# Kernel tuning notes

Measured on AMD Instinct MI355X. Metric: run time of the kernel, lower is better.

## Reference

```python
import jax, jax.numpy as jnp
import numpy as np

N = 50000      # nodes per graph batch (per siamese side)
E = 500000     # edges per side
F_IN = 128     # input_channels
H = 128        # hidden_channels
OUT = 2        # output_channels
G = 512        # number of graphs in the batch


def setup_inputs() -> dict:
    key = jax.random.key(0)
    ks = jax.random.split(key, 16)

    def lin_w(k, fan_in, shape):
        lim = 1.0 / np.sqrt(fan_in)
        return jax.random.uniform(k, shape, jnp.float32, -lim, lim)

    return {
        "x1": jax.random.normal(ks[0], (N, F_IN), jnp.float32),
        "x2": jax.random.normal(ks[1], (N, F_IN), jnp.float32),
        "edge_index1": jax.random.randint(ks[2], (2, E), 0, N, jnp.int32),
        "edge_index2": jax.random.randint(ks[3], (2, E), 0, N, jnp.int32),
        "batch1": jnp.sort(jax.random.randint(ks[4], (N,), 0, G, jnp.int32)),
        "batch2": jnp.sort(jax.random.randint(ks[5], (N,), 0, G, jnp.int32)),
        "W1": lin_w(ks[6], F_IN, (F_IN, H)), "b1": jnp.zeros((H,), jnp.float32),
        "W2": lin_w(ks[7], H, (H, H)),       "b2": jnp.zeros((H,), jnp.float32),
        "W3": lin_w(ks[8], H, (H, H)),       "b3": jnp.zeros((H,), jnp.float32),
        "Wc1": lin_w(ks[9], 2 * H, (2 * H, 4 * H)), "bc1": jnp.zeros((4 * H,), jnp.float32),
        "Wc2": lin_w(ks[10], 4 * H, (4 * H, 2 * H)), "bc2": jnp.zeros((2 * H,), jnp.float32),
        "Wc3": lin_w(ks[11], 2 * H, (2 * H, OUT)),   "bc3": jnp.zeros((OUT,), jnp.float32),
        "num_graphs": G,
    }


def _gcn_layer(x, W, b, src, dst, dinv):
    # PyG GCNConv: linear transform, then deg^{-1/2} A_hat deg^{-1/2} aggregation + bias
    h = x @ W
    msg = h[src] * (dinv[src] * dinv[dst])[:, None]   # [E+N, H]
    return jax.ops.segment_sum(msg, dst, num_segments=x.shape[0]) + b


def _forward_once(x, edge_index, batch, W1, b1, W2, b2, W3, b3, num_graphs):
    n = x.shape[0]
    loop = jnp.arange(n, dtype=edge_index.dtype)
    src = jnp.concatenate([edge_index[0], loop])      # add self-loops
    dst = jnp.concatenate([edge_index[1], loop])
    deg = jax.ops.segment_sum(jnp.ones_like(dst, dtype=x.dtype), dst, num_segments=n)
    dinv = jax.lax.rsqrt(deg)                          # deg >= 1 due to self-loops
    h = jax.nn.relu(_gcn_layer(x, W1, b1, src, dst, dinv))
    h = jax.nn.relu(_gcn_layer(h, W2, b2, src, dst, dinv))
    h = _gcn_layer(h, W3, b3, src, dst, dinv)
    # global_mean_pool over batch indices
    s = jax.ops.segment_sum(h, batch, num_segments=num_graphs)
    cnt = jax.ops.segment_sum(jnp.ones((n,), x.dtype), batch, num_segments=num_graphs)
    return s / jnp.maximum(cnt, 1.0)[:, None]


def reference(x1, x2, edge_index1, edge_index2, batch1, batch2,
              W1, b1, W2, b2, W3, b3, Wc1, bc1, Wc2, bc2, Wc3, bc3, num_graphs):
    g1 = _forward_once(x1, edge_index1, batch1, W1, b1, W2, b2, W3, b3, num_graphs)
    g2 = _forward_once(x2, edge_index2, batch2, W1, b1, W2, b2, W3, b3, num_graphs)
    z = jnp.concatenate([g1, g2], axis=1)             # [G, 2H]
    z = jax.nn.relu(z @ Wc1 + bc1)
    z = jax.nn.relu(z @ Wc2 + bc2)
    # dropout p=0.5 is identity at eval time
    return z @ Wc3 + bc3                               # [G, OUT]
```

## Files before the change

kernel.cpp:

```cpp
#include <hip/hip_runtime.h>
#include <math.h>

#define N_NODES 50000
#define E_EDGES 500000
#define HDIM    128
#define OUTC    2
#define NGRAPH  512

typedef _Float16 f16x8 __attribute__((ext_vector_type(8)));
typedef float    f32x4 __attribute__((ext_vector_type(4)));

__global__ void k_prep(int* __restrict__ zA, int nA, int* __restrict__ zB, int nB,
                       const float* __restrict__ W1, const float* __restrict__ W2,
                       _Float16* __restrict__ w1hi, _Float16* __restrict__ w1lo,
                       _Float16* __restrict__ w2hi, _Float16* __restrict__ w2lo) {
    int i = blockIdx.x * blockDim.x + threadIdx.x;
    int stride = gridDim.x * blockDim.x;
    for (int j = i; j < nA; j += stride) zA[j] = 0;
    for (int j = i; j < nB; j += stride) zB[j] = 0;
    for (int j = i; j < 128 * 128; j += stride) {
        int n = j >> 7, k = j & 127;
        float v = W1[k * 128 + n];
        _Float16 h = (_Float16)v;
        w1hi[j] = h; w1lo[j] = (_Float16)(v - (float)h);
        v = W2[k * 128 + n];
        h = (_Float16)v;
        w2hi[j] = h; w2lo[j] = (_Float16)(v - (float)h);
    }
}

__global__ void k_hist(const int* __restrict__ d0, const int* __restrict__ d1,
                       int ecnt, int off1, int* __restrict__ cnt) {
    int i = blockIdx.x * blockDim.x + threadIdx.x;
    int stride = gridDim.x * blockDim.x;
    for (; i < ecnt; i += stride) {
        int d = (i < E_EDGES) ? d0[i] : d1[i - E_EDGES] + off1;
        atomicAdd(&cnt[d], 1);
    }
}

__global__ void k_scan_a(const int* __restrict__ cnt, int* __restrict__ excl,
                         int* __restrict__ blksum, float* __restrict__ dinv,
                         const int* __restrict__ bt0, const int* __restrict__ bt1,
                         int goff0, int nn, int nside, float* __restrict__ cnt_g) {
    __shared__ int s[512];
    int t = threadIdx.x;
    int i = blockIdx.x * 512 + t;
    int v = 0;
    if (i < nn) {
        v = cnt[i];
        dinv[i] = 1.0f / sqrtf((float)(v + 1));
        int g = (i < nside) ? bt0[i] + goff0 : bt1[i - nside] + NGRAPH;
        atomicAdd(&cnt_g[g], 1.0f);
    }
    s[t] = v; __syncthreads();
    for (int off = 1; off < 512; off <<= 1) {
        int add = (t >= off) ? s[t - off] : 0;
        __syncthreads();
        s[t] += add;
        __syncthreads();
    }
    if (i < nn) excl[i] = s[t] - v;
    if (t == 511) blksum[blockIdx.x] = s[511];
}

__global__ void k_scan_b(int* __restrict__ blksum, int nb) {
    __shared__ int s[512];
    int t = threadIdx.x;
    int v = (t < nb) ? blksum[t] : 0;
    s[t] = v; __syncthreads();
    for (int off = 1; off < 512; off <<= 1) {
        int add = (t >= off) ? s[t - off] : 0;
        __syncthreads();
        s[t] += add;
        __syncthreads();
    }
    if (t < nb) blksum[t] = s[t] - v;
}

__global__ void k_scan_c(int* __restrict__ excl, const int* __restrict__ blksum,
                         int nn, int tot) {
    int t = threadIdx.x;
    int i = blockIdx.x * 512 + t;
    if (i < nn) excl[i] += blksum[blockIdx.x];
    if (i == 0) excl[nn] = tot;
}

__global__ void k_fill(const int* __restrict__ s0, const int* __restrict__ s1,
                       const int* __restrict__ d0, const int* __restrict__ d1,
                       int ecnt, int off1,
                       const int* __restrict__ row_ptr, int* __restrict__ fill_cnt,
                       const float* __restrict__ dinv, int2* __restrict__ edges) {
    int i = blockIdx.x * blockDim.x + threadIdx.x;
    int stride = gridDim.x * blockDim.x;
    for (; i < ecnt; i += stride) {
        int d, sg;
        if (i < E_EDGES) { sg = s0[i]; d = d0[i]; }
        else             { sg = s1[i - E_EDGES] + off1; d = d1[i - E_EDGES] + off1; }
        int p = atomicAdd(&fill_cnt[d], 1);
        float w = dinv[sg] * dinv[d];
        edges[row_ptr[d] + p] = make_int2(sg, __float_as_int(w));
    }
}

__device__ inline void cvt8(const float4& p, const float4& q, f16x8& h, f16x8& l) {
    float v[8] = {p.x, p.y, p.z, p.w, q.x, q.y, q.z, q.w};
#pragma unroll
    for (int i = 0; i < 8; i++) {
        _Float16 hh = (_Float16)v[i];
        h[i] = hh;
        l[i] = (_Float16)(v[i] - (float)hh);
    }
}

template <int ASRC>
__global__ __launch_bounds__(256) void k_gemm_split(
        const float* __restrict__ A0f, const float* __restrict__ A1f, int nside,
        const _Float16* __restrict__ Ahi, const _Float16* __restrict__ Alo,
        const _Float16* __restrict__ Bhi, const _Float16* __restrict__ Blo,
        float* __restrict__ C, int M) {
    __shared__ _Float16 sA[2][128][40];
    __shared__ _Float16 sB[2][128][40];
    int tid = threadIdx.x;
    int wave = tid >> 6, lane = tid & 63;
    int wm = (wave >> 1) * 64;
    int wn = (wave & 1) * 64;
    int quad = lane >> 4, fm = lane & 15;
    int row0 = blockIdx.x * 128;

    int lr = tid >> 2;
    int lk = (tid & 3) * 8;

    f32x4 acc[4][4] = {};
    const float4 z4 = make_float4(0.f, 0.f, 0.f, 0.f);

    for (int kc = 0; kc < 128; kc += 32) {
        int r1 = row0 + lr, r2 = row0 + lr + 64;
        bool ok1 = r1 < M, ok2 = r2 < M;
        f16x8 ah1, al1, ah2, al2;
        if (ASRC == 1) {
            const float* p1 = (r1 < nside) ? A0f + (size_t)r1 * 128
                                           : A1f + (size_t)(r1 - nside) * 128;
            const float* p2 = (r2 < nside) ? A0f + (size_t)r2 * 128
                                           : A1f + (size_t)(r2 - nside) * 128;
            float4 a = ok1 ? *(const float4*)(p1 + kc + lk) : z4;
            float4 b = ok1 ? *(const float4*)(p1 + kc + lk + 4) : z4;
            float4 c = ok2 ? *(const float4*)(p2 + kc + lk) : z4;
            float4 d = ok2 ? *(const float4*)(p2 + kc + lk + 4) : z4;
            cvt8(a, b, ah1, al1);
            cvt8(c, d, ah2, al2);
        } else {
            const f16x8 zf = {};
            ah1 = ok1 ? *(const f16x8*)(Ahi + (size_t)r1 * 128 + kc + lk) : zf;
            al1 = ok1 ? *(const f16x8*)(Alo + (size_t)r1 * 128 + kc + lk) : zf;
            ah2 = ok2 ? *(const f16x8*)(Ahi + (size_t)r2 * 128 + kc + lk) : zf;
            al2 = ok2 ? *(const f16x8*)(Alo + (size_t)r2 * 128 + kc + lk) : zf;
        }
        f16x8 bh1 = *(const f16x8*)(Bhi + (size_t)lr * 128 + kc + lk);
        f16x8 bl1 = *(const f16x8*)(Blo + (size_t)lr * 128 + kc + lk);
        f16x8 bh2 = *(const f16x8*)(Bhi + (size_t)(lr + 64) * 128 + kc + lk);
        f16x8 bl2 = *(const f16x8*)(Blo + (size_t)(lr + 64) * 128 + kc + lk);
        __syncthreads();
        *(f16x8*)&sA[0][lr][lk]      = ah1;
        *(f16x8*)&sA[1][lr][lk]      = al1;
        *(f16x8*)&sA[0][lr + 64][lk] = ah2;
        *(f16x8*)&sA[1][lr + 64][lk] = al2;
        *(f16x8*)&sB[0][lr][lk]      = bh1;
        *(f16x8*)&sB[1][lr][lk]      = bl1;
        *(f16x8*)&sB[0][lr + 64][lk] = bh2;
        *(f16x8*)&sB[1][lr + 64][lk] = bl2;
        __syncthreads();

        f16x8 afh[4], afl[4], bfh[4], bfl[4];
#pragma unroll
        for (int mi = 0; mi < 4; mi++) {
            afh[mi] = *(const f16x8*)&sA[0][wm + mi * 16 + fm][quad * 8];
            afl[mi] = *(const f16x8*)&sA[1][wm + mi * 16 + fm][quad * 8];
        }
#pragma unroll
        for (int ni = 0; ni < 4; ni++) {
            bfh[ni] = *(const f16x8*)&sB[0][wn + ni * 16 + fm][quad * 8];
            bfl[ni] = *(const f16x8*)&sB[1][wn + ni * 16 + fm][quad * 8];
        }
#pragma unroll
        for (int mi = 0; mi < 4; mi++)
#pragma unroll
            for (int ni = 0; ni < 4; ni++) {
                acc[mi][ni] = __builtin_amdgcn_mfma_f32_16x16x32_f16(afh[mi], bfh[ni], acc[mi][ni], 0, 0, 0);
                acc[mi][ni] = __builtin_amdgcn_mfma_f32_16x16x32_f16(afh[mi], bfl[ni], acc[mi][ni], 0, 0, 0);
                acc[mi][ni] = __builtin_amdgcn_mfma_f32_16x16x32_f16(afl[mi], bfh[ni], acc[mi][ni], 0, 0, 0);
            }
    }

#pragma unroll
    for (int mi = 0; mi < 4; mi++)
#pragma unroll
        for (int reg = 0; reg < 4; reg++) {
            int r = row0 + wm + mi * 16 + quad * 4 + reg;
            if (r >= M) continue;
#pragma unroll
            for (int ni = 0; ni < 4; ni++)
                C[(size_t)r * 128 + wn + ni * 16 + fm] = acc[mi][ni][reg];
        }
}

__global__ __launch_bounds__(256) void k_gemm(
        const float* __restrict__ A, const float* __restrict__ B,
        const float* __restrict__ bias, float* __restrict__ C,
        int M, int Nn, int K, int ldc, int act) {
    __shared__ float As[16][64];
    __shared__ float Bs[16][68];
    int tid = threadIdx.x;
    int tx = tid & 15, ty = tid >> 4;
    int row0 = blockIdx.x * 64, col0 = blockIdx.y * 64;
    float acc[4][4] = {};
    int arow = tid >> 2;
    int acol = (tid & 3) * 4;
    int brow = tid >> 4;
    int bcol = (tid & 15) * 4;

    for (int k0 = 0; k0 < K; k0 += 16) {
        float4 av = make_float4(0.f, 0.f, 0.f, 0.f);
        int ar = row0 + arow;
        if (ar < M) av = *(const float4*)(A + (size_t)ar * K + k0 + acol);
        As[acol + 0][arow] = av.x;
        As[acol + 1][arow] = av.y;
        As[acol + 2][arow] = av.z;
        As[acol + 3][arow] = av.w;

        float4 bv = make_float4(0.f, 0.f, 0.f, 0.f);
        const float* Brow = B + (size_t)(k0 + brow) * Nn;
        int bc = col0 + bcol;
        if (bc + 3 < Nn) {
            bv = *(const float4*)(Brow + bc);
        } else {
            if (bc     < Nn) bv.x = Brow[bc];
            if (bc + 1 < Nn) bv.y = Brow[bc + 1];
            if (bc + 2 < Nn) bv.z = Brow[bc + 2];
        }
        Bs[brow][bcol + 0] = bv.x;
        Bs[brow][bcol + 1] = bv.y;
        Bs[brow][bcol + 2] = bv.z;
        Bs[brow][bcol + 3] = bv.w;
        __syncthreads();

#pragma unroll
        for (int k = 0; k < 16; k++) {
            float4 a = *(const float4*)&As[k][ty * 4];
            float4 b = *(const float4*)&Bs[k][tx * 4];
            acc[0][0] += a.x * b.x; acc[0][1] += a.x * b.y; acc[0][2] += a.x * b.z; acc[0][3] += a.x * b.w;
            acc[1][0] += a.y * b.x; acc[1][1] += a.y * b.y; acc[1][2] += a.y * b.z; acc[1][3] += a.y * b.w;
            acc[2][0] += a.z * b.x; acc[2][1] += a.z * b.y; acc[2][2] += a.z * b.z; acc[2][3] += a.z * b.w;
            acc[3][0] += a.w * b.x; acc[3][1] += a.w * b.y; acc[3][2] += a.w * b.z; acc[3][3] += a.w * b.w;
        }
        __syncthreads();
    }

#pragma unroll
    for (int i = 0; i < 4; i++) {
        int r = row0 + ty * 4 + i;
        if (r >= M) continue;
#pragma unroll
        for (int j = 0; j < 4; j++) {
            int c = col0 + tx * 4 + j;
            if (c >= Nn) continue;
            float v = acc[i][j];
            if (bias) v += bias[c];
            if (act) v = fmaxf(v, 0.0f);
            C[(size_t)r * ldc + c] = v;
        }
    }
}

__global__ __launch_bounds__(256) void k_gemm_pool(
        const float* __restrict__ pool, const float* __restrict__ cnt_g,
        const float* __restrict__ W, const float* __restrict__ bias,
        float* __restrict__ zcat) {
    __shared__ float As[16][64];
    __shared__ float Bs[16][68];
    int side = blockIdx.z;
    const float* A = pool + (size_t)side * NGRAPH * HDIM;
    const float* cg = cnt_g + side * NGRAPH;
    int tid = threadIdx.x;
    int tx = tid & 15, ty = tid >> 4;
    int row0 = blockIdx.x * 64, col0 = blockIdx.y * 64;
    float acc[4][4] = {};
    int arow = tid >> 2;
    int acol = (tid & 3) * 4;
    int brow = tid >> 4;
    int bcol = (tid & 15) * 4;

    for (int k0 = 0; k0 < 128; k0 += 16) {
        int ar = row0 + arow;
        float sc = 1.0f / fmaxf(cg[ar], 1.0f);
        float4 av = *(const float4*)(A + (size_t)ar * 128 + k0 + acol);
        As[acol + 0][arow] = av.x * sc;
        As[acol + 1][arow] = av.y * sc;
        As[acol + 2][arow] = av.z * sc;
        As[acol + 3][arow] = av.w * sc;

        float4 bv = *(const float4*)(W + (size_t)(k0 + brow) * 128 + col0 + bcol);
        Bs[brow][bcol + 0] = bv.x;
        Bs[brow][bcol + 1] = bv.y;
        Bs[brow][bcol + 2] = bv.z;
        Bs[brow][bcol + 3] = bv.w;
        __syncthreads();

#pragma unroll
        for (int k = 0; k < 16; k++) {
            float4 a = *(const float4*)&As[k][ty * 4];
            float4 b = *(const float4*)&Bs[k][tx * 4];
            acc[0][0] += a.x * b.x; acc[0][1] += a.x * b.y; acc[0][2] += a.x * b.z; acc[0][3] += a.x * b.w;
            acc[1][0] += a.y * b.x; acc[1][1] += a.y * b.y; acc[1][2] += a.y * b.z; acc[1][3] += a.y * b.w;
            acc[2][0] += a.z * b.x; acc[2][1] += a.z * b.y; acc[2][2] += a.z * b.z; acc[2][3] += a.z * b.w;
            acc[3][0] += a.w * b.x; acc[3][1] += a.w * b.y; acc[3][2] += a.w * b.z; acc[3][3] += a.w * b.w;
        }
        __syncthreads();
    }

#pragma unroll
    for (int i = 0; i < 4; i++) {
        int r = row0 + ty * 4 + i;
#pragma unroll
        for (int j = 0; j < 4; j++) {
            int c = col0 + tx * 4 + j;
            zcat[(size_t)r * 256 + side * 128 + c] = acc[i][j] + bias[c];
        }
    }
}

template <int MODE, int PACK>
__global__ __launch_bounds__(256) void k_agg(
        const float* __restrict__ H, const float* __restrict__ dinv,
        const int* __restrict__ row_ptr, const int2* __restrict__ edges,
        const float* __restrict__ bias,
        _Float16* __restrict__ outHi, _Float16* __restrict__ outLo,
        float* __restrict__ outF,
        const int* __restrict__ bt0, const int* __restrict__ bt1,
        int goff0, int nnodes, int nside, float* __restrict__ pool) {
    int wave = threadIdx.x >> 6, lane = threadIdx.x & 63;
    int node = blockIdx.x * 4 + wave;
    if (node >= nnodes) return;

    float di = dinv[node];
    float2 hv = ((const float2*)(H + (size_t)node * HDIM))[lane];
    float wself = di * di;
    float ax = hv.x * wself;
    float ay = hv.y * wself;

    int rs = __builtin_amdgcn_readfirstlane(row_ptr[node]);
    int re = __builtin_amdgcn_readfirstlane(row_ptr[node + 1]);

    int2 E0, E1, E2, E3, E4, E5, E6, E7;
    if (rs < re) {
        int nrem = re - rs, m = nrem - 1;
        E0 = edges[rs];
        E1 = edges[rs + (1 < nrem ? 1 : m)];
        E2 = edges[rs + (2 < nrem ? 2 : m)];
        E3 = edges[rs + (3 < nrem ? 3 : m)];
        E4 = edges[rs + (4 < nrem ? 4 : m)];
        E5 = edges[rs + (5 < nrem ? 5 : m)];
        E6 = edges[rs + (6 < nrem ? 6 : m)];
        E7 = edges[rs + (7 < nrem ? 7 : m)];
    }

    for (int base = rs; base < re; base += 8) {
        int nb = base + 8;
        int2 P0 = E0, P1 = E1, P2 = E2, P3 = E3, P4 = E4, P5 = E5, P6 = E6, P7 = E7;
        if (nb < re) {
            int nr2 = re - nb, m2 = nr2 - 1;
            P0 = edges[nb];
            P1 = edges[nb + (1 < nr2 ? 1 : m2)];
            P2 = edges[nb + (2 < nr2 ? 2 : m2)];
            P3 = edges[nb + (3 < nr2 ? 3 : m2)];
            P4 = edges[nb + (4 < nr2 ? 4 : m2)];
            P5 = edges[nb + (5 < nr2 ? 5 : m2)];
            P6 = edges[nb + (6 < nr2 ? 6 : m2)];
            P7 = edges[nb + (7 < nr2 ? 7 : m2)];
        }

        float2 v0 = ((const float2*)(H + (size_t)E0.x * HDIM))[lane];
        float2 v1 = ((const float2*)(H + (size_t)E1.x * HDIM))[lane];
        float2 v2 = ((const float2*)(H + (size_t)E2.x * HDIM))[lane];
        float2 v3 = ((const float2*)(H + (size_t)E3.x * HDIM))[lane];
        float2 v4 = ((const float2*)(H + (size_t)E4.x * HDIM))[lane];
        float2 v5 = ((const float2*)(H + (size_t)E5.x * HDIM))[lane];
        float2 v6 = ((const float2*)(H + (size_t)E6.x * HDIM))[lane];
        float2 v7 = ((const float2*)(H + (size_t)E7.x * HDIM))[lane];

        int nrem = re - base;
        float w0 = __int_as_float(E0.y);
        float w1 = 1 < nrem ? __int_as_float(E1.y) : 0.f;
        float w2 = 2 < nrem ? __int_as_float(E2.y) : 0.f;
        float w3 = 3 < nrem ? __int_as_float(E3.y) : 0.f;
        float w4 = 4 < nrem ? __int_as_float(E4.y) : 0.f;
        float w5 = 5 < nrem ? __int_as_float(E5.y) : 0.f;
        float w6 = 6 < nrem ? __int_as_float(E6.y) : 0.f;
        float w7 = 7 < nrem ? __int_as_float(E7.y) : 0.f;

        ax = fmaf(v0.x, w0, ax); ay = fmaf(v0.y, w0, ay);
        ax = fmaf(v1.x, w1, ax); ay = fmaf(v1.y, w1, ay);
        ax = fmaf(v2.x, w2, ax); ay = fmaf(v2.y, w2, ay);
        ax = fmaf(v3.x, w3, ax); ay = fmaf(v3.y, w3, ay);
        ax = fmaf(v4.x, w4, ax); ay = fmaf(v4.y, w4, ay);
        ax = fmaf(v5.x, w5, ax); ay = fmaf(v5.y, w5, ay);
        ax = fmaf(v6.x, w6, ax); ay = fmaf(v6.y, w6, ay);
        ax = fmaf(v7.x, w7, ax); ay = fmaf(v7.y, w7, ay);

        E0 = P0; E1 = P1; E2 = P2; E3 = P3;
        E4 = P4; E5 = P5; E6 = P6; E7 = P7;
    }

    if (MODE == 2) {
        int g = (node < nside) ? bt0[node] + goff0 : bt1[node - nside] + NGRAPH;
        float* p = pool + (size_t)g * HDIM + lane * 2;
        atomicAdd(p,     ax);
        atomicAdd(p + 1, ay);
    } else {
        float ox = fmaxf(ax + bias[lane * 2],     0.0f);
        float oy = fmaxf(ay + bias[lane * 2 + 1], 0.0f);
        if (PACK) {
            _Float16 hx = (_Float16)ox, hy = (_Float16)oy;
            _Float16 lx = (_Float16)(ox - (float)hx), ly = (_Float16)(oy - (float)hy);
            union { _Float16 h[2]; unsigned u; } ph, pl;
            ph.h[0] = hx; ph.h[1] = hy;
            pl.h[0] = lx; pl.h[1] = ly;
            ((unsigned*)(outHi + (size_t)node * HDIM))[lane] = ph.u;
            ((unsigned*)(outLo + (size_t)node * HDIM))[lane] = pl.u;
        } else {
            ((float2*)(outF + (size_t)node * HDIM))[lane] = make_float2(ox, oy);
        }
    }
}

extern "C" void kernel_launch(void* const* d_in, const int* in_sizes, int n_in,
                              void* d_out, int out_size, void* d_ws, size_t ws_size,
                              hipStream_t stream) {
    (void)in_sizes; (void)n_in; (void)out_size;

    const float* x[2]  = {(const float*)d_in[0], (const float*)d_in[1]};
    const int*   ei[2] = {(const int*)d_in[2], (const int*)d_in[3]};
    const int*   bt[2] = {(const int*)d_in[4], (const int*)d_in[5]};
    const float* W1  = (const float*)d_in[6];  const float* b1  = (const float*)d_in[7];
    const float* W2  = (const float*)d_in[8];  const float* b2  = (const float*)d_in[9];
    const float* W3  = (const float*)d_in[10]; const float* b3  = (const float*)d_in[11];
    const float* Wc1 = (const float*)d_in[12]; const float* bc1 = (const float*)d_in[13];
    const float* Wc2 = (const float*)d_in[14]; const float* bc2 = (const float*)d_in[15];
    const float* Wc3 = (const float*)d_in[16]; const float* bc3 = (const float*)d_in[17];
    float* out = (float*)d_out;

    const bool batched = ws_size >= 120ull * 1000 * 1000;
    const int NN = batched ? 2 * N_NODES : N_NODES;
    const int NE = batched ? 2 * E_EDGES : E_EDGES;

    char* ws = (char*)d_ws;
    size_t off = 0;
    auto carve = [&](size_t bytes) -> char* {
        char* p = ws + off;
        off += (bytes + 255) & ~(size_t)255;
        return p;
    };

    int*   edge_cnt = (int*)  carve((size_t)NN * 4);
    int*   fill_cnt = (int*)  carve((size_t)NN * 4);
    float* pool_s   = (float*)carve((size_t)2 * NGRAPH * HDIM * 4);
    float* cnt_g    = (float*)carve((size_t)2 * NGRAPH * 4);
    float* dinv     = (float*)carve((size_t)NN * 4);
    int*   row_ptr  = (int*)  carve((size_t)(NN + 1) * 4);
    int2*  edges    = (int2*) carve((size_t)NE * 8);
    int*   blksum   = (int*)  carve(1024 * 4);
    _Float16* wt    = (_Float16*)carve(4 * 128 * 128 * 2);
    _Float16* hS    = (_Float16*)carve((size_t)NN * HDIM * 4);
    float* hA       = (float*)carve((size_t)NN * HDIM * 4);
    float* zcat     = (float*)carve((size_t)NGRAPH * 2 * HDIM * 4);
    float* z1       = (float*)carve((size_t)NGRAPH * 4 * HDIM * 4);
    float* z2       = (float*)carve((size_t)NGRAPH * 2 * HDIM * 4);

    _Float16* w1hi = wt;
    _Float16* w1lo = wt + 128 * 128;
    _Float16* w2hi = wt + 2 * 128 * 128;
    _Float16* w2lo = wt + 3 * 128 * 128;
    _Float16* hShi = hS;
    _Float16* hSlo = hS + (size_t)NN * HDIM;
    float*    hSf  = (float*)hS;

    int zeroA_words = (int)(((char*)pool_s - (char*)edge_cnt) / 4);
    int zeroB_words = (int)(((char*)dinv   - (char*)pool_s)   / 4);

    const int gblk = (NN + 127) / 128;

    if (batched) {
        const int nscan = (2 * N_NODES + 511) / 512;
        const int ablk  = (2 * N_NODES + 3) / 4;

        k_prep<<<512, 256, 0, stream>>>(edge_cnt, zeroA_words, (int*)pool_s, zeroB_words,
                                        W1, W2, w1hi, w1lo, w2hi, w2lo);
        k_hist<<<1024, 256, 0, stream>>>(ei[0] + E_EDGES, ei[1] + E_EDGES,
                                         2 * E_EDGES, N_NODES, edge_cnt);
        k_scan_a<<<nscan, 512, 0, stream>>>(edge_cnt, row_ptr, blksum, dinv,
                                            bt[0], bt[1], 0, 2 * N_NODES, N_NODES, cnt_g);
        k_scan_b<<<1, 512, 0, stream>>>(blksum, nscan);
        k_scan_c<<<nscan, 512, 0, stream>>>(row_ptr, blksum, 2 * N_NODES, 2 * E_EDGES);
        k_fill<<<1024, 256, 0, stream>>>(ei[0], ei[1], ei[0] + E_EDGES, ei[1] + E_EDGES,
                                         2 * E_EDGES, N_NODES, row_ptr, fill_cnt, dinv, edges);

        k_gemm_split<1><<<gblk, 256, 0, stream>>>(x[0], x[1], N_NODES,
                                                  nullptr, nullptr, w1hi, w1lo, hA, 2 * N_NODES);
        k_agg<0, 1><<<ablk, 256, 0, stream>>>(hA, dinv, row_ptr, edges, b1,
                                              hShi, hSlo, nullptr, bt[0], bt[1], 0,
                                              2 * N_NODES, N_NODES, nullptr);
        k_gemm_split<0><<<gblk, 256, 0, stream>>>(nullptr, nullptr, 0,
                                                  hShi, hSlo, w2hi, w2lo, hA, 2 * N_NODES);
        k_agg<0, 0><<<ablk, 256, 0, stream>>>(hA, dinv, row_ptr, edges, b2,
                                              nullptr, nullptr, hSf, bt[0], bt[1], 0,
                                              2 * N_NODES, N_NODES, nullptr);
        k_agg<2, 0><<<ablk, 256, 0, stream>>>(hSf, dinv, row_ptr, edges, nullptr,
                                              nullptr, nullptr, nullptr, bt[0], bt[1], 0,
                                              2 * N_NODES, N_NODES, pool_s);
    } else {
        const int nscan = (N_NODES + 511) / 512;
        const int ablk  = (N_NODES + 3) / 4;

        k_prep<<<512, 256, 0, stream>>>(edge_cnt, zeroA_words, (int*)pool_s, zeroB_words,
                                        W1, W2, w1hi, w1lo, w2hi, w2lo);
        for (int s = 0; s < 2; ++s) {
            const int* esrc = ei[s];
            const int* edst = ei[s] + E_EDGES;
            int goff = s * NGRAPH;

            if (s == 1)
                k_prep<<<512, 256, 0, stream>>>(edge_cnt, zeroA_words, (int*)pool_s, 0,
                                                W1, W2, w1hi, w1lo, w2hi, w2lo);
            k_hist<<<512, 256, 0, stream>>>(edst, edst, E_EDGES, 0, edge_cnt);
            k_scan_a<<<nscan, 512, 0, stream>>>(edge_cnt, row_ptr, blksum, dinv,
                                                bt[s], bt[s], goff, N_NODES, N_NODES, cnt_g);
            k_scan_b<<<1, 512, 0, stream>>>(blksum, nscan);
            k_scan_c<<<nscan, 512, 0, stream>>>(row_ptr, blksum, N_NODES, E_EDGES);
            k_fill<<<512, 256, 0, stream>>>(esrc, esrc, edst, edst, E_EDGES, 0,
                                            row_ptr, fill_cnt, dinv, edges);

            k_gemm_split<1><<<gblk, 256, 0, stream>>>(x[s], x[s], N_NODES,
                                                      nullptr, nullptr, w1hi, w1lo, hA, N_NODES);
            k_agg<0, 1><<<ablk, 256, 0, stream>>>(hA, dinv, row_ptr, edges, b1,
                                                  hShi, hSlo, nullptr, bt[s], bt[s], goff,
                                                  N_NODES, N_NODES, nullptr);
            k_gemm_split<0><<<gblk, 256, 0, stream>>>(nullptr, nullptr, 0,
                                                      hShi, hSlo, w2hi, w2lo, hA, N_NODES);
            k_agg<0, 0><<<ablk, 256, 0, stream>>>(hA, dinv, row_ptr, edges, b2,
                                                  nullptr, nullptr, hSf, bt[s], bt[s], goff,
                                                  N_NODES, N_NODES, nullptr);
            k_agg<2, 0><<<ablk, 256, 0, stream>>>(hSf, dinv, row_ptr, edges, nullptr,
                                                  nullptr, nullptr, nullptr, bt[s], bt[s], goff,
                                                  N_NODES, N_NODES, pool_s);
        }
    }

    k_gemm_pool<<<dim3(NGRAPH / 64, 2, 2), 256, 0, stream>>>(pool_s, cnt_g, W3, b3, zcat);

    k_gemm<<<dim3(NGRAPH / 64, (4 * HDIM) / 64), 256, 0, stream>>>(zcat, Wc1, bc1, z1, NGRAPH, 4 * HDIM, 2 * HDIM, 4 * HDIM, 1);
    k_gemm<<<dim3(NGRAPH / 64, (2 * HDIM) / 64), 256, 0, stream>>>(z1, Wc2, bc2, z2, NGRAPH, 2 * HDIM, 4 * HDIM, 2 * HDIM, 1);
    k_gemm<<<dim3(NGRAPH / 64, 1), 256, 0, stream>>>(z2, Wc3, bc3, out, NGRAPH, OUTC, 2 * HDIM, OUTC, 0);
}
```

Measured before the change: 676.6 us.

## Replace third-layer node aggregation with edge-sweep pooling keyed by graph id

Layer 3 with mean pooling is linear, so the per-node aggregation followed by a pool is replaced by one sweep. Each wave walks a contiguous chunk of CSR edges, which are tagged with the destination graph id written by k_fill, and flushes atomics into the pool only when the graph id changes. Self-loop terms go through a separate node sweep. k_fill now writes positions through a cursor array seeded by the scan, removing the row_ptr read. Zeroing moves to hipMemsetAsync, and k_agg drops its edge-prefetch double buffering. The costs are an extra gdst array to write and read, and atomics on graph boundaries.

```diff
diff --git a/kernel.cpp b/kernel.cpp
--- a/kernel.cpp
+++ b/kernel.cpp
@@ -10,14 +10,11 @@
 typedef _Float16 f16x8 __attribute__((ext_vector_type(8)));
 typedef float    f32x4 __attribute__((ext_vector_type(4)));
 
-__global__ void k_prep(int* __restrict__ zA, int nA, int* __restrict__ zB, int nB,
-                       const float* __restrict__ W1, const float* __restrict__ W2,
+__global__ void k_prep(const float* __restrict__ W1, const float* __restrict__ W2,
                        _Float16* __restrict__ w1hi, _Float16* __restrict__ w1lo,
                        _Float16* __restrict__ w2hi, _Float16* __restrict__ w2lo) {
     int i = blockIdx.x * blockDim.x + threadIdx.x;
     int stride = gridDim.x * blockDim.x;
-    for (int j = i; j < nA; j += stride) zA[j] = 0;
-    for (int j = i; j < nB; j += stride) zB[j] = 0;
     for (int j = i; j < 128 * 128; j += stride) {
         int n = j >> 7, k = j & 127;
         float v = W1[k * 128 + n];
@@ -79,27 +76,39 @@
 }
 
 __global__ void k_scan_c(int* __restrict__ excl, const int* __restrict__ blksum,
-                         int nn, int tot) {
+                         int* __restrict__ cursor, int nn, int tot) {
     int t = threadIdx.x;
     int i = blockIdx.x * 512 + t;
-    if (i < nn) excl[i] += blksum[blockIdx.x];
+    if (i < nn) {
+        int v = excl[i] + blksum[blockIdx.x];
+        excl[i] = v;
+        cursor[i] = v;
+    }
     if (i == 0) excl[nn] = tot;
 }
 
 __global__ void k_fill(const int* __restrict__ s0, const int* __restrict__ s1,
                        const int* __restrict__ d0, const int* __restrict__ d1,
-                       int ecnt, int off1,
-                       const int* __restrict__ row_ptr, int* __restrict__ fill_cnt,
-                       const float* __restrict__ dinv, int2* __restrict__ edges) {
+                       int ecnt, int off1, int goff0,
+                       const int* __restrict__ bt0, const int* __restrict__ bt1,
+                       int* __restrict__ cursor,
+                       const float* __restrict__ dinv, int2* __restrict__ edges,
+                       int* __restrict__ gdst) {
     int i = blockIdx.x * blockDim.x + threadIdx.x;
     int stride = gridDim.x * blockDim.x;
     for (; i < ecnt; i += stride) {
-        int d, sg;
-        if (i < E_EDGES) { sg = s0[i]; d = d0[i]; }
-        else             { sg = s1[i - E_EDGES] + off1; d = d1[i - E_EDGES] + off1; }
-        int p = atomicAdd(&fill_cnt[d], 1);
+        int d, sg, g;
+        if (i < E_EDGES) {
+            int dl = d0[i];
+            sg = s0[i]; d = dl; g = bt0[dl] + goff0;
+        } else {
+            int dl = d1[i - E_EDGES];
+            sg = s1[i - E_EDGES] + off1; d = dl + off1; g = bt1[dl] + NGRAPH;
+        }
+        int p = atomicAdd(&cursor[d], 1);
         float w = dinv[sg] * dinv[d];
-        edges[row_ptr[d] + p] = make_int2(sg, __float_as_int(w));
+        edges[p] = make_int2(sg, __float_as_int(w));
+        gdst[p] = g;
     }
 }
 
@@ -329,15 +338,13 @@
     }
 }
 
-template <int MODE, int PACK>
+template <int PACK>
 __global__ __launch_bounds__(256) void k_agg(
         const float* __restrict__ H, const float* __restrict__ dinv,
         const int* __restrict__ row_ptr, const int2* __restrict__ edges,
         const float* __restrict__ bias,
         _Float16* __restrict__ outHi, _Float16* __restrict__ outLo,
-        float* __restrict__ outF,
-        const int* __restrict__ bt0, const int* __restrict__ bt1,
-        int goff0, int nnodes, int nside, float* __restrict__ pool) {
+        float* __restrict__ outF, int nnodes) {
     int wave = threadIdx.x >> 6, lane = threadIdx.x & 63;
     int node = blockIdx.x * 4 + wave;
     if (node >= nnodes) return;
@@ -351,34 +358,23 @@
     int rs = __builtin_amdgcn_readfirstlane(row_ptr[node]);
     int re = __builtin_amdgcn_readfirstlane(row_ptr[node + 1]);
 
-    int2 E0, E1, E2, E3, E4, E5, E6, E7;
-    if (rs < re) {
-        int nrem = re - rs, m = nrem - 1;
-        E0 = edges[rs];
-        E1 = edges[rs + (1 < nrem ? 1 : m)];
-        E2 = edges[rs + (2 < nrem ? 2 : m)];
-        E3 = edges[rs + (3 < nrem ? 3 : m)];
-        E4 = edges[rs + (4 < nrem ? 4 : m)];
-        E5 = edges[rs + (5 < nrem ? 5 : m)];
-        E6 = edges[rs + (6 < nrem ? 6 : m)];
-        E7 = edges[rs + (7 < nrem ? 7 : m)];
-    }
-
     for (int base = rs; base < re; base += 8) {
-        int nb = base + 8;
-        int2 P0 = E0, P1 = E1, P2 = E2, P3 = E3, P4 = E4, P5 = E5, P6 = E6, P7 = E7;
-        if (nb < re) {
-            int nr2 = re - nb, m2 = nr2 - 1;
-            P0 = edges[nb];
-            P1 = edges[nb + (1 < nr2 ? 1 : m2)];
-            P2 = edges[nb + (2 < nr2 ? 2 : m2)];
-            P3 = edges[nb + (3 < nr2 ? 3 : m2)];
-            P4 = edges[nb + (4 < nr2 ? 4 : m2)];
-            P5 = edges[nb + (5 < nr2 ? 5 : m2)];
-            P6 = edges[nb + (6 < nr2 ? 6 : m2)];
-            P7 = edges[nb + (7 < nr2 ? 7 : m2)];
-        }
-
+        int nrem = re - base, m = nrem - 1;
+        int i1 = 1 < nrem ? 1 : m;
+        int i2 = 2 < nrem ? 2 : m;
+        int i3 = 3 < nrem ? 3 : m;
+        int i4 = 4 < nrem ? 4 : m;
+        int i5 = 5 < nrem ? 5 : m;
+        int i6 = 6 < nrem ? 6 : m;
+        int i7 = 7 < nrem ? 7 : m;
+        int2 E0 = edges[base];
+        int2 E1 = edges[base + i1];
+        int2 E2 = edges[base + i2];
+        int2 E3 = edges[base + i3];
+        int2 E4 = edges[base + i4];
+        int2 E5 = edges[base + i5];
+        int2 E6 = edges[base + i6];
+        int2 E7 = edges[base + i7];
         float2 v0 = ((const float2*)(H + (size_t)E0.x * HDIM))[lane];
         float2 v1 = ((const float2*)(H + (size_t)E1.x * HDIM))[lane];
         float2 v2 = ((const float2*)(H + (size_t)E2.x * HDIM))[lane];
@@ -387,8 +383,6 @@
         float2 v5 = ((const float2*)(H + (size_t)E5.x * HDIM))[lane];
         float2 v6 = ((const float2*)(H + (size_t)E6.x * HDIM))[lane];
         float2 v7 = ((const float2*)(H + (size_t)E7.x * HDIM))[lane];
-
-        int nrem = re - base;
         float w0 = __int_as_float(E0.y);
         float w1 = 1 < nrem ? __int_as_float(E1.y) : 0.f;
         float w2 = 2 < nrem ? __int_as_float(E2.y) : 0.f;
@@ -397,7 +391,6 @@
         float w5 = 5 < nrem ? __int_as_float(E5.y) : 0.f;
         float w6 = 6 < nrem ? __int_as_float(E6.y) : 0.f;
         float w7 = 7 < nrem ? __int_as_float(E7.y) : 0.f;
-
         ax = fmaf(v0.x, w0, ax); ay = fmaf(v0.y, w0, ay);
         ax = fmaf(v1.x, w1, ax); ay = fmaf(v1.y, w1, ay);
         ax = fmaf(v2.x, w2, ax); ay = fmaf(v2.y, w2, ay);
@@ -406,30 +399,134 @@
         ax = fmaf(v5.x, w5, ax); ay = fmaf(v5.y, w5, ay);
         ax = fmaf(v6.x, w6, ax); ay = fmaf(v6.y, w6, ay);
         ax = fmaf(v7.x, w7, ax); ay = fmaf(v7.y, w7, ay);
-
-        E0 = P0; E1 = P1; E2 = P2; E3 = P3;
-        E4 = P4; E5 = P5; E6 = P6; E7 = P7;
-    }
-
-    if (MODE == 2) {
-        int g = (node < nside) ? bt0[node] + goff0 : bt1[node - nside] + NGRAPH;
-        float* p = pool + (size_t)g * HDIM + lane * 2;
-        atomicAdd(p,     ax);
-        atomicAdd(p + 1, ay);
+    }
+
+    float ox = fmaxf(ax + bias[lane * 2],     0.0f);
+    float oy = fmaxf(ay + bias[lane * 2 + 1], 0.0f);
+    if (PACK) {
+        _Float16 hx = (_Float16)ox, hy = (_Float16)oy;
+        _Float16 lx = (_Float16)(ox - (float)hx), ly = (_Float16)(oy - (float)hy);
+        union { _Float16 h[2]; unsigned u; } ph, pl;
+        ph.h[0] = hx; ph.h[1] = hy;
+        pl.h[0] = lx; pl.h[1] = ly;
+        ((unsigned*)(outHi + (size_t)node * HDIM))[lane] = ph.u;
+        ((unsigned*)(outLo + (size_t)node * HDIM))[lane] = pl.u;
     } else {
-        float ox = fmaxf(ax + bias[lane * 2],     0.0f);
-        float oy = fmaxf(ay + bias[lane * 2 + 1], 0.0f);
-        if (PACK) {
-            _Float16 hx = (_Float16)ox, hy = (_Float16)oy;
-            _Float16 lx = (_Float16)(ox - (float)hx), ly = (_Float16)(oy - (float)hy);
-            union { _Float16 h[2]; unsigned u; } ph, pl;
-            ph.h[0] = hx; ph.h[1] = hy;
-            pl.h[0] = lx; pl.h[1] = ly;
-            ((unsigned*)(outHi + (size_t)node * HDIM))[lane] = ph.u;
-            ((unsigned*)(outLo + (size_t)node * HDIM))[lane] = pl.u;
-        } else {
-            ((float2*)(outF + (size_t)node * HDIM))[lane] = make_float2(ox, oy);
-        }
+        ((float2*)(outF + (size_t)node * HDIM))[lane] = make_float2(ox, oy);
+    }
+}
+
+__global__ __launch_bounds__(256) void k_sweep3(
+        const float* __restrict__ H, const int2* __restrict__ edges,
+        const int* __restrict__ gdst, const float* __restrict__ dinv,
+        const int* __restrict__ bt0, const int* __restrict__ bt1,
+        int goff0, int nnodes, int nside, int nedges,
+        float* __restrict__ pool) {
+    int lane = threadIdx.x & 63;
+    int wid = blockIdx.x * 4 + (threadIdx.x >> 6);
+    int ewaves = (nedges + 63) >> 6;
+
+    float ax = 0.f, ay = 0.f;
+
+    if (wid < ewaves) {
+        int e0 = wid << 6;
+        int e1 = e0 + 64; if (e1 > nedges) e1 = nedges;
+        int gcur = __builtin_amdgcn_readfirstlane(gdst[e0]);
+        for (int base = e0; base < e1; base += 8) {
+            int nrem = e1 - base, m = nrem - 1;
+            int i1 = 1 < nrem ? 1 : m;
+            int i2 = 2 < nrem ? 2 : m;
+            int i3 = 3 < nrem ? 3 : m;
+            int i4 = 4 < nrem ? 4 : m;
+            int i5 = 5 < nrem ? 5 : m;
+            int i6 = 6 < nrem ? 6 : m;
+            int i7 = 7 < nrem ? 7 : m;
+            int2 E0 = edges[base];
+            int2 E1 = edges[base + i1];
+            int2 E2 = edges[base + i2];
+            int2 E3 = edges[base + i3];
+            int2 E4 = edges[base + i4];
+            int2 E5 = edges[base + i5];
+            int2 E6 = edges[base + i6];
+            int2 E7 = edges[base + i7];
+            int g0 = __builtin_amdgcn_readfirstlane(gdst[base]);
+            int g1 = __builtin_amdgcn_readfirstlane(gdst[base + i1]);
+            int g2 = __builtin_amdgcn_readfirstlane(gdst[base + i2]);
+            int g3 = __builtin_amdgcn_readfirstlane(gdst[base + i3]);
+            int g4 = __builtin_amdgcn_readfirstlane(gdst[base + i4]);
+            int g5 = __builtin_amdgcn_readfirstlane(gdst[base + i5]);
+            int g6 = __builtin_amdgcn_readfirstlane(gdst[base + i6]);
+            int g7 = __builtin_amdgcn_readfirstlane(gdst[base + i7]);
+            float2 v0 = ((const float2*)(H + (size_t)E0.x * HDIM))[lane];
+            float2 v1 = ((const float2*)(H + (size_t)E1.x * HDIM))[lane];
+            float2 v2 = ((const float2*)(H + (size_t)E2.x * HDIM))[lane];
+            float2 v3 = ((const float2*)(H + (size_t)E3.x * HDIM))[lane];
+            float2 v4 = ((const float2*)(H + (size_t)E4.x * HDIM))[lane];
+            float2 v5 = ((const float2*)(H + (size_t)E5.x * HDIM))[lane];
+            float2 v6 = ((const float2*)(H + (size_t)E6.x * HDIM))[lane];
+            float2 v7 = ((const float2*)(H + (size_t)E7.x * HDIM))[lane];
+            float w0 = __int_as_float(E0.y);
+            float w1 = 1 < nrem ? __int_as_float(E1.y) : 0.f;
+            float w2 = 2 < nrem ? __int_as_float(E2.y) : 0.f;
+            float w3 = 3 < nrem ? __int_as_float(E3.y) : 0.f;
+            float w4 = 4 < nrem ? __int_as_float(E4.y) : 0.f;
+            float w5 = 5 < nrem ? __int_as_float(E5.y) : 0.f;
+            float w6 = 6 < nrem ? __int_as_float(E6.y) : 0.f;
+            float w7 = 7 < nrem ? __int_as_float(E7.y) : 0.f;
+
+            if ((g0 | g1 | g2 | g3 | g4 | g5 | g6 | g7) ==
+                (g0 & g1 & g2 & g3 & g4 & g5 & g6 & g7) && g0 == gcur) {
+                ax = fmaf(v0.x, w0, ax); ay = fmaf(v0.y, w0, ay);
+                ax = fmaf(v1.x, w1, ax); ay = fmaf(v1.y, w1, ay);
+                ax = fmaf(v2.x, w2, ax); ay = fmaf(v2.y, w2, ay);
+                ax = fmaf(v3.x, w3, ax); ay = fmaf(v3.y, w3, ay);
+                ax = fmaf(v4.x, w4, ax); ay = fmaf(v4.y, w4, ay);
+                ax = fmaf(v5.x, w5, ax); ay = fmaf(v5.y, w5, ay);
+                ax = fmaf(v6.x, w6, ax); ay = fmaf(v6.y, w6, ay);
+                ax = fmaf(v7.x, w7, ax); ay = fmaf(v7.y, w7, ay);
+            } else {
+                int   gg[8] = {g0, g1, g2, g3, g4, g5, g6, g7};
+                float wx[8] = {w0, w1, w2, w3, w4, w5, w6, w7};
+                float2 vv[8] = {v0, v1, v2, v3, v4, v5, v6, v7};
+#pragma unroll
+                for (int j = 0; j < 8; j++) {
+                    if (wx[j] != 0.f && gg[j] != gcur) {
+                        float* p = pool + (size_t)gcur * HDIM + lane * 2;
+                        atomicAdd(p, ax); atomicAdd(p + 1, ay);
+                        ax = 0.f; ay = 0.f;
+                        gcur = gg[j];
+                    }
+                    ax = fmaf(vv[j].x, wx[j], ax);
+                    ay = fmaf(vv[j].y, wx[j], ay);
+                }
+            }
+        }
+        float* p = pool + (size_t)gcur * HDIM + lane * 2;
+        atomicAdd(p, ax); atomicAdd(p + 1, ay);
+    } else {
+        int wid2 = wid - ewaves;
+        int n0 = wid2 << 6;
+        if (n0 >= nnodes) return;
+        int n1 = n0 + 64; if (n1 > nnodes) n1 = nnodes;
+        int gcur = (n0 < nside) ? bt0[n0] + goff0 : bt1[n0 - nside] + NGRAPH;
+        gcur = __builtin_amdgcn_readfirstlane(gcur);
+        for (int n = n0; n < n1; n++) {
+            int g = (n < nside) ? bt0[n] + goff0 : bt1[n - nside] + NGRAPH;
+            g = __builtin_amdgcn_readfirstlane(g);
+            float dn = dinv[n];
+            float w = dn * dn;
+            float2 v = ((const float2*)(H + (size_t)n * HDIM))[lane];
+            if (g != gcur) {
+                float* p = pool + (size_t)gcur * HDIM + lane * 2;
+                atomicAdd(p, ax); atomicAdd(p + 1, ay);
+                ax = 0.f; ay = 0.f;
+                gcur = g;
+            }
+            ax = fmaf(v.x, w, ax);
+            ay = fmaf(v.y, w, ay);
+        }
+        float* p = pool + (size_t)gcur * HDIM + lane * 2;
+        atomicAdd(p, ax); atomicAdd(p + 1, ay);
     }
 }
 
@@ -462,12 +559,13 @@
     };
 
     int*   edge_cnt = (int*)  carve((size_t)NN * 4);
-    int*   fill_cnt = (int*)  carve((size_t)NN * 4);
+    int*   cursor   = (int*)  carve((size_t)NN * 4);
     float* pool_s   = (float*)carve((size_t)2 * NGRAPH * HDIM * 4);
     float* cnt_g    = (float*)carve((size_t)2 * NGRAPH * 4);
     float* dinv     = (float*)carve((size_t)NN * 4);
     int*   row_ptr  = (int*)  carve((size_t)(NN + 1) * 4);
     int2*  edges    = (int2*) carve((size_t)NE * 8);
+    int*   gdst     = (int*)  carve((size_t)NE * 4);
     int*   blksum   = (int*)  carve(1024 * 4);
     _Float16* wt    = (_Float16*)carve(4 * 128 * 128 * 2);
     _Float16* hS    = (_Float16*)carve((size_t)NN * HDIM * 4);
@@ -484,74 +582,69 @@
     _Float16* hSlo = hS + (size_t)NN * HDIM;
     float*    hSf  = (float*)hS;
 
-    int zeroA_words = (int)(((char*)pool_s - (char*)edge_cnt) / 4);
-    int zeroB_words = (int)(((char*)dinv   - (char*)pool_s)   / 4);
-
     const int gblk = (NN + 127) / 128;
+    const size_t poolz = (size_t)2 * NGRAPH * HDIM * 4 + (size_t)2 * NGRAPH * 4;
+
+    hipMemsetAsync(pool_s, 0, poolz, stream);
+    k_prep<<<64, 256, 0, stream>>>(W1, W2, w1hi, w1lo, w2hi, w2lo);
 
     if (batched) {
         const int nscan = (2 * N_NODES + 511) / 512;
         const int ablk  = (2 * N_NODES + 3) / 4;
-
-        k_prep<<<512, 256, 0, stream>>>(edge_cnt, zeroA_words, (int*)pool_s, zeroB_words,
-                                        W1, W2, w1hi, w1lo, w2hi, w2lo);
+        const int swaves = ((2 * E_EDGES + 63) >> 6) + ((2 * N_NODES + 63) >> 6);
+        const int sblk = (swaves + 3) / 4;
+
+        hipMemsetAsync(edge_cnt, 0, (size_t)NN * 4, stream);
         k_hist<<<1024, 256, 0, stream>>>(ei[0] + E_EDGES, ei[1] + E_EDGES,
                                          2 * E_EDGES, N_NODES, edge_cnt);
         k_scan_a<<<nscan, 512, 0, stream>>>(edge_cnt, row_ptr, blksum, dinv,
                                             bt[0], bt[1], 0, 2 * N_NODES, N_NODES, cnt_g);
         k_scan_b<<<1, 512, 0, stream>>>(blksum, nscan);
-        k_scan_c<<<nscan, 512, 0, stream>>>(row_ptr, blksum, 2 * N_NODES, 2 * E_EDGES);
+        k_scan_c<<<nscan, 512, 0, stream>>>(row_ptr, blksum, cursor, 2 * N_NODES, 2 * E_EDGES);
         k_fill<<<1024, 256, 0, stream>>>(ei[0], ei[1], ei[0] + E_EDGES, ei[1] + E_EDGES,
-                                         2 * E_EDGES, N_NODES, row_ptr, fill_cnt, dinv, edges);
+                                         2 * E_EDGES, N_NODES, 0, bt[0], bt[1],
+                                         cursor, dinv, edges, gdst);
 
         k_gemm_split<1><<<gblk, 256, 0, stream>>>(x[0], x[1], N_NODES,
                                                   nullptr, nullptr, w1hi, w1lo, hA, 2 * N_NODES);
-        k_agg<0, 1><<<ablk, 256, 0, stream>>>(hA, dinv, row_ptr, edges, b1,
-                                              hShi, hSlo, nullptr, bt[0], bt[1], 0,
-                                              2 * N_NODES, N_NODES, nullptr);
+        k_agg<1><<<ablk, 256, 0, stream>>>(hA, dinv, row_ptr, edges, b1,
+                                           hShi, hSlo, nullptr, 2 * N_NODES);
         k_gemm_split<0><<<gblk, 256, 0, stream>>>(nullptr, nullptr, 0,
                                                   hShi, hSlo, w2hi, w2lo, hA, 2 * N_NODES);
-        k_agg<0, 0><<<ablk, 256, 0, stream>>>(hA, dinv, row_ptr, edges, b2,
-                                              nullptr, nullptr, hSf, bt[0], bt[1], 0,
-                                              2 * N_NODES, N_NODES, nullptr);
-        k_agg<2, 0><<<ablk, 256, 0, stream>>>(hSf, dinv, row_ptr, edges, nullptr,
-                                              nullptr, nullptr, nullptr, bt[0], bt[1], 0,
-                                              2 * N_NODES, N_NODES, pool_s);
+        k_agg<0><<<ablk, 256, 0, stream>>>(hA, dinv, row_ptr, edges, b2,
+                                           nullptr, nullptr, hSf, 2 * N_NODES);
+        k_sweep3<<<sblk, 256, 0, stream>>>(hSf, edges, gdst, dinv, bt[0], bt[1],
+                                           0, 2 * N_NODES, N_NODES, 2 * E_EDGES, pool_s);
     } else {
         const int nscan = (N_NODES + 511) / 512;
         const int ablk  = (N_NODES + 3) / 4;
-
-        k_prep<<<512, 256, 0, stream>>>(edge_cnt, zeroA_words, (int*)pool_s, zeroB_words,
-                                        W1, W2, w1hi, w1lo, w2hi, w2lo);
+        const int swaves = ((E_EDGES + 63) >> 6) + ((N_NODES + 63) >> 6);
+        const int sblk = (swaves + 3) / 4;
+
         for (int s = 0; s < 2; ++s) {
             const int* esrc = ei[s];
             const int* edst = ei[s] + E_EDGES;
             int goff = s * NGRAPH;
 
-            if (s == 1)
-                k_prep<<<512, 256, 0, stream>>>(edge_cnt, zeroA_words, (int*)pool_s, 0,
-                                                W1, W2, w1hi, w1lo, w2hi, w2lo);
+            hipMemsetAsync(edge_cnt, 0, (size_t)NN * 4, stream);
             k_hist<<<512, 256, 0, stream>>>(edst, edst, E_EDGES, 0, edge_cnt);
             k_scan_a<<<nscan, 512, 0, stream>>>(edge_cnt, row_ptr, blksum, dinv,
                                                 bt[s], bt[s], goff, N_NODES, N_NODES, cnt_g);
             k_scan_b<<<1, 512, 0, stream>>>(blksum, nscan);
-            k_scan_c<<<nscan, 512, 0, stream>>>(row_ptr, blksum, N_NODES, E_EDGES);
-            k_fill<<<512, 256, 0, stream>>>(esrc, esrc, edst, edst, E_EDGES, 0,
-                                            row_ptr, fill_cnt, dinv, edges);
+            k_scan_c<<<nscan, 512, 0, stream>>>(row_ptr, blksum, cursor, N_NODES, E_EDGES);
+            k_fill<<<512, 256, 0, stream>>>(esrc, esrc, edst, edst, E_EDGES, 0, goff,
+                                            bt[s], bt[s], cursor, dinv, edges, gdst);
 
             k_gemm_split<1><<<gblk, 256, 0, stream>>>(x[s], x[s], N_NODES,
                                                       nullptr, nullptr, w1hi, w1lo, hA, N_NODES);
-            k_agg<0, 1><<<ablk, 256, 0, stream>>>(hA, dinv, row_ptr, edges, b1,
-                                                  hShi, hSlo, nullptr, bt[s], bt[s], goff,
-                                                  N_NODES, N_NODES, nullptr);
+            k_agg<1><<<ablk, 256, 0, stream>>>(hA, dinv, row_ptr, edges, b1,
+                                               hShi, hSlo, nullptr, N_NODES);
             k_gemm_split<0><<<gblk, 256, 0, stream>>>(nullptr, nullptr, 0,
                                                       hShi, hSlo, w2hi, w2lo, hA, N_NODES);
-            k_agg<0, 0><<<ablk, 256, 0, stream>>>(hA, dinv, row_ptr, edges, b2,
-                                                  nullptr, nullptr, hSf, bt[s], bt[s], goff,
-                                                  N_NODES, N_NODES, nullptr);
-            k_agg<2, 0><<<ablk, 256, 0, stream>>>(hSf, dinv, row_ptr, edges, nullptr,
-                                                  nullptr, nullptr, nullptr, bt[s], bt[s], goff,
-                                                  N_NODES, N_NODES, pool_s);
+            k_agg<0><<<ablk, 256, 0, stream>>>(hA, dinv, row_ptr, edges, b2,
+                                               nullptr, nullptr, hSf, N_NODES);
+            k_sweep3<<<sblk, 256, 0, stream>>>(hSf, edges, gdst, dinv, bt[s], bt[s],
+                                               goff, N_NODES, N_NODES, E_EDGES, pool_s);
         }
     }
 
```

Result: no change. 678.3 us (+0.2%).
